# Kernel tuning notes

Hardware: AMD Instinct MI355X
Metric: run time of the kernel (lower is better)

Reference implementation:

```python
import jax, jax.numpy as jnp
import numpy as np

M, D, I, E, TOPK = 2048, 1024, 2048, 8, 2

def setup_inputs() -> dict:
    key = jax.random.key(0)
    k1, k2, k3, k4 = jax.random.split(key, 4)
    x = jax.random.normal(k1, (M, D), dtype=jnp.float32)
    w13 = jax.random.normal(k2, (E, 2 * I, D), dtype=jnp.float32) * 0.02
    w2 = jax.random.normal(k3, (E, D, I), dtype=jnp.float32) * 0.02
    expert_indices = jax.random.randint(k4, (M, TOPK), 0, E, dtype=jnp.int64)
    return {"x": x, "w13": w13, "w2": w2, "expert_indices": expert_indices}

def reference(x, w13, w2, expert_indices):
    # Faithful to the 'gpt-fast' math: per (token, slot) SiLU-gated expert FFN.
    # Instead of gathering per-token weight copies (huge), compute each expert's
    # FFN densely over all tokens, then gather the selected expert output.
    inter = w2.shape[2]

    def per_expert(w13_e, w2_e):
        h = jnp.einsum('md,nd->mn', x, w13_e)          # [M, 2I]
        x1, x3 = h[:, :inter], h[:, inter:]
        return jnp.einsum('mi,di->md', jax.nn.silu(x1) * x3, w2_e)  # [M, D]

    outs = jax.vmap(per_expert)(w13, w2)               # [E, M, D]
    outs = jnp.transpose(outs, (1, 0, 2))              # [M, E, D]
    # out[t, a] = outs[t, expert_indices[t, a]]
    idx = expert_indices[..., None]                    # [M, TOPK, 1]
    return jnp.take_along_axis(outs, idx, axis=1)      # [M, TOPK, D]
```

## Files before the change

### kernel.cpp

```cpp
#include <hip/hip_runtime.h>
#include <hip/hip_bf16.h>
#include <cstdint>
#include <cstddef>

#define DDIM  1024
#define IDIM  2048
#define NEXP  8
#define NPAIR 4096
#define MAXTILE 40

typedef __attribute__((ext_vector_type(8))) short short8;
typedef __attribute__((ext_vector_type(4))) float floatx4;
typedef __attribute__((ext_vector_type(4))) float fvec4;

__device__ inline short8 pack8v(fvec4 a, fvec4 b) {
    union { short8 s8; __hip_bfloat162 h[4]; } u;
    u.h[0] = __float22bfloat162_rn(float2{a.x, a.y});
    u.h[1] = __float22bfloat162_rn(float2{a.z, a.w});
    u.h[2] = __float22bfloat162_rn(float2{b.x, b.y});
    u.h[3] = __float22bfloat162_rn(float2{b.z, b.w});
    return u.s8;
}

__device__ inline void gload_lds16(const unsigned short* g, unsigned short* l) {
    __builtin_amdgcn_global_load_lds((const __attribute__((address_space(1))) void*)g,
                                     (__attribute__((address_space(3))) void*)l, 16, 0, 0);
}

__launch_bounds__(256)
__global__ void cvt_all(const fvec4* __restrict__ x, const fvec4* __restrict__ w13,
                        const fvec4* __restrict__ w2,
                        uint4* __restrict__ xb, uint4* __restrict__ w13b,
                        uint4* __restrict__ w2b) {
    const int t = threadIdx.x;
    for (int job = blockIdx.x; job < 6400; job += gridDim.x) {
        const fvec4* src; uint4* dst; int cbase;
        if (job < 4096)      { src = w13; dst = w13b; cbase = job << 10; }
        else if (job < 6144) { src = w2;  dst = w2b;  cbase = (job - 4096) << 10; }
        else                 { src = x;   dst = xb;   cbase = (job - 6144) << 10; }
        const int c0 = cbase + t;
        fvec4 a0 = __builtin_nontemporal_load(src + 2 * (c0 + 0));
        fvec4 b0 = __builtin_nontemporal_load(src + 2 * (c0 + 0) + 1);
        fvec4 a1 = __builtin_nontemporal_load(src + 2 * (c0 + 256));
        fvec4 b1 = __builtin_nontemporal_load(src + 2 * (c0 + 256) + 1);
        fvec4 a2 = __builtin_nontemporal_load(src + 2 * (c0 + 512));
        fvec4 b2 = __builtin_nontemporal_load(src + 2 * (c0 + 512) + 1);
        fvec4 a3 = __builtin_nontemporal_load(src + 2 * (c0 + 768));
        fvec4 b3 = __builtin_nontemporal_load(src + 2 * (c0 + 768) + 1);
        __builtin_amdgcn_sched_barrier(0);
        short8 p0 = pack8v(a0, b0);
        short8 p1 = pack8v(a1, b1);
        short8 p2 = pack8v(a2, b2);
        short8 p3 = pack8v(a3, b3);
        dst[c0 + 0]   = *(uint4*)&p0;
        dst[c0 + 256] = *(uint4*)&p1;
        dst[c0 + 512] = *(uint4*)&p2;
        dst[c0 + 768] = *(uint4*)&p3;
    }
}

__global__ void route_kernel(const int* __restrict__ eidx,
                             int4* __restrict__ tbl,
                             int* __restrict__ slot_q) {
    __shared__ int cnt[NEXP];
    __shared__ int cur[NEXP];
    const int t = threadIdx.x;
    if (t < NEXP) cnt[t] = 0;
    __syncthreads();
    for (int q = t; q < NPAIR; q += 1024) atomicAdd(&cnt[eidx[q]], 1);
    __syncthreads();
    if (t == 0) {
        int s = 0, nt = 0;
        for (int e = 0; e < NEXP; e++) {
            cur[e] = s;
            for (int mb = 0; mb < cnt[e]; mb += 128)
                tbl[nt++] = int4{e, mb, s, cnt[e]};
            s += cnt[e];
        }
        for (; nt < MAXTILE; nt++) tbl[nt] = int4{0, 0, 0, 0};
    }
    __syncthreads();
    for (int q = t; q < NPAIR; q += 1024) {
        int e = eidx[q];
        int pos = atomicAdd(&cur[e], 1);
        slot_q[pos] = q;
    }
}

__launch_bounds__(256)
__global__ void gemm1_swiglu(const unsigned short* __restrict__ xb,
                             const unsigned short* __restrict__ w13b,
                             const int4* __restrict__ tbl,
                             const int* __restrict__ slot_q,
                             unsigned short* __restrict__ pbuf) {
    const int4 tt = tbl[blockIdx.y];
    const int e = tt.x, mbase = tt.y, off0 = tt.z, ne = tt.w;
    if (mbase >= ne) return;
    const int n0 = blockIdx.x * 64;

    __shared__ __align__(16) unsigned short As[2][128 * 64];
    __shared__ __align__(16) unsigned short Bs[2][128 * 64];

    const int t    = threadIdx.x;
    const int lane = t & 63;
    const int wid  = t >> 6;

    const int rr = t >> 3;
    const int g  = (t & 7) ^ (rr & 7);
    const unsigned short* pA[4];
    const unsigned short* pB[4];
    const unsigned short* wb1 = w13b + (size_t)e * (2 * IDIM) * DDIM;
    #pragma unroll
    for (int c = 0; c < 4; c++) {
        int row = c * 32 + rr;
        int sl = mbase + row; if (sl > ne - 1) sl = ne - 1;
        pA[c] = xb + (size_t)(slot_q[off0 + sl] >> 1) * DDIM + g * 8;
        int wrow = (row < 64) ? (n0 + row) : (IDIM + n0 + (row - 64));
        pB[c] = wb1 + (size_t)wrow * DDIM + g * 8;
    }
    const int lo = wid * 512;

    const int wm = wid >> 1, wn = wid & 1;
    const int quad = lane >> 4, l16 = lane & 15;
    const int rsw = l16 & 7;
    const int co0 = (quad ^ rsw) * 8;
    const int co1 = ((quad + 4) ^ rsw) * 8;

    floatx4 acc1[4][2], acc3[4][2];
    #pragma unroll
    for (int i = 0; i < 4; i++)
        #pragma unroll
        for (int j = 0; j < 2; j++) {
            acc1[i][j] = floatx4{0.f, 0.f, 0.f, 0.f};
            acc3[i][j] = floatx4{0.f, 0.f, 0.f, 0.f};
        }

    #pragma unroll
    for (int c = 0; c < 4; c++) {
        gload_lds16(pA[c], &As[0][lo + c * 2048]);
        gload_lds16(pB[c], &Bs[0][lo + c * 2048]);
    }
    __builtin_amdgcn_sched_barrier(0);

    int cur = 0;
    for (int it = 0; it < DDIM / 64; ++it) {
        if (it + 1 < DDIM / 64) {
            const int ko = (it + 1) * 64;
            #pragma unroll
            for (int c = 0; c < 4; c++) {
                gload_lds16(pA[c] + ko, &As[cur ^ 1][lo + c * 2048]);
                gload_lds16(pB[c] + ko, &Bs[cur ^ 1][lo + c * 2048]);
            }
            __builtin_amdgcn_sched_barrier(0);
            asm volatile("s_waitcnt vmcnt(8)" ::: "memory");
        } else {
            asm volatile("s_waitcnt vmcnt(0)" ::: "memory");
        }
        __builtin_amdgcn_s_barrier();
        __builtin_amdgcn_sched_barrier(0);

        __builtin_amdgcn_s_setprio(1);
        #pragma unroll
        for (int h = 0; h < 2; ++h) {
            const int co = h ? co1 : co0;
            short8 af[4], b1f[2], b3f[2];
            #pragma unroll
            for (int mi = 0; mi < 4; mi++)
                af[mi] = *(short8*)&As[cur][(wm * 64 + mi * 16 + l16) * 64 + co];
            #pragma unroll
            for (int ni = 0; ni < 2; ni++) {
                b1f[ni] = *(short8*)&Bs[cur][(wn * 32 + ni * 16 + l16) * 64 + co];
                b3f[ni] = *(short8*)&Bs[cur][(64 + wn * 32 + ni * 16 + l16) * 64 + co];
            }
            #pragma unroll
            for (int mi = 0; mi < 4; mi++)
                #pragma unroll
                for (int ni = 0; ni < 2; ni++) {
                    acc1[mi][ni] = __builtin_amdgcn_mfma_f32_16x16x32_bf16(af[mi], b1f[ni], acc1[mi][ni], 0, 0, 0);
                    acc3[mi][ni] = __builtin_amdgcn_mfma_f32_16x16x32_bf16(af[mi], b3f[ni], acc3[mi][ni], 0, 0, 0);
                }
        }
        __builtin_amdgcn_s_setprio(0);
        __builtin_amdgcn_s_barrier();
        __builtin_amdgcn_sched_barrier(0);
        cur ^= 1;
    }

    #pragma unroll
    for (int mi = 0; mi < 4; mi++) {
        #pragma unroll
        for (int ni = 0; ni < 2; ni++) {
            const int col = n0 + wn * 32 + ni * 16 + l16;
            #pragma unroll
            for (int rw = 0; rw < 4; rw++) {
                const int s2 = mbase + wm * 64 + mi * 16 + quad * 4 + rw;
                if (s2 < ne) {
                    float v1 = acc1[mi][ni][rw];
                    float v3 = acc3[mi][ni][rw];
                    float pv = v1 / (1.f + __expf(-v1)) * v3;
                    __hip_bfloat16 pb = __float2bfloat16(pv);
                    pbuf[(size_t)(off0 + s2) * IDIM + col] = *(unsigned short*)&pb;
                }
            }
        }
    }
}

__launch_bounds__(256)
__global__ void gemm2_out(const unsigned short* __restrict__ pbuf,
                          const unsigned short* __restrict__ w2b,
                          const int4* __restrict__ tbl,
                          const int* __restrict__ slot_q,
                          float* __restrict__ out) {
    const int4 tt = tbl[blockIdx.y];
    const int e = tt.x, mbase = tt.y, off0 = tt.z, ne = tt.w;
    if (mbase >= ne) return;
    const int n0 = blockIdx.x * 64;

    __shared__ __align__(16) unsigned short As[2][128 * 64];
    __shared__ __align__(16) unsigned short Bs[2][64 * 64];

    const int t    = threadIdx.x;
    const int lane = t & 63;
    const int wid  = t >> 6;

    const int rr = t >> 3;
    const int g  = (t & 7) ^ (rr & 7);
    const unsigned short* pA[4];
    const unsigned short* pB[2];
    const unsigned short* wb = w2b + (size_t)e * DDIM * IDIM;
    #pragma unroll
    for (int c = 0; c < 4; c++) {
        int row = c * 32 + rr;
        int sl = mbase + row; if (sl > ne - 1) sl = ne - 1;
        pA[c] = pbuf + (size_t)(off0 + sl) * IDIM + g * 8;
    }
    #pragma unroll
    for (int c = 0; c < 2; c++) {
        int row = c * 32 + rr;
        pB[c] = wb + (size_t)(n0 + row) * IDIM + g * 8;
    }
    const int lo = wid * 512;

    const int wm = wid >> 1, wn = wid & 1;
    const int quad = lane >> 4, l16 = lane & 15;
    const int rsw = l16 & 7;
    const int co0 = (quad ^ rsw) * 8;
    const int co1 = ((quad + 4) ^ rsw) * 8;

    floatx4 acc[4][2];
    #pragma unroll
    for (int i = 0; i < 4; i++)
        #pragma unroll
        for (int j = 0; j < 2; j++) acc[i][j] = floatx4{0.f, 0.f, 0.f, 0.f};

    #pragma unroll
    for (int c = 0; c < 4; c++)
        gload_lds16(pA[c], &As[0][lo + c * 2048]);
    #pragma unroll
    for (int c = 0; c < 2; c++)
        gload_lds16(pB[c], &Bs[0][lo + c * 2048]);
    __builtin_amdgcn_sched_barrier(0);

    int cur = 0;
    for (int it = 0; it < IDIM / 64; ++it) {
        if (it + 1 < IDIM / 64) {
            const int ko = (it + 1) * 64;
            #pragma unroll
            for (int c = 0; c < 4; c++)
                gload_lds16(pA[c] + ko, &As[cur ^ 1][lo + c * 2048]);
            #pragma unroll
            for (int c = 0; c < 2; c++)
                gload_lds16(pB[c] + ko, &Bs[cur ^ 1][lo + c * 2048]);
            __builtin_amdgcn_sched_barrier(0);
            asm volatile("s_waitcnt vmcnt(6)" ::: "memory");
        } else {
            asm volatile("s_waitcnt vmcnt(0)" ::: "memory");
        }
        __builtin_amdgcn_s_barrier();
        __builtin_amdgcn_sched_barrier(0);

        __builtin_amdgcn_s_setprio(1);
        #pragma unroll
        for (int h = 0; h < 2; ++h) {
            const int co = h ? co1 : co0;
            short8 af[4], bf[2];
            #pragma unroll
            for (int mi = 0; mi < 4; mi++)
                af[mi] = *(short8*)&As[cur][(wm * 64 + mi * 16 + l16) * 64 + co];
            #pragma unroll
            for (int ni = 0; ni < 2; ni++)
                bf[ni] = *(short8*)&Bs[cur][(wn * 32 + ni * 16 + l16) * 64 + co];
            #pragma unroll
            for (int mi = 0; mi < 4; mi++)
                #pragma unroll
                for (int ni = 0; ni < 2; ni++)
                    acc[mi][ni] = __builtin_amdgcn_mfma_f32_16x16x32_bf16(af[mi], bf[ni], acc[mi][ni], 0, 0, 0);
        }
        __builtin_amdgcn_s_setprio(0);
        __builtin_amdgcn_s_barrier();
        __builtin_amdgcn_sched_barrier(0);
        cur ^= 1;
    }

    #pragma unroll
    for (int mi = 0; mi < 4; mi++) {
        #pragma unroll
        for (int rw = 0; rw < 4; rw++) {
            const int s2 = mbase + wm * 64 + mi * 16 + quad * 4 + rw;
            if (s2 < ne) {
                const int qq = slot_q[off0 + s2];
                float* orow = out + (size_t)qq * DDIM;
                #pragma unroll
                for (int ni = 0; ni < 2; ni++)
                    orow[n0 + wn * 32 + ni * 16 + l16] = acc[mi][ni][rw];
            }
        }
    }
}

extern "C" void kernel_launch(void* const* d_in, const int* in_sizes, int n_in,
                              void* d_out, int out_size, void* d_ws, size_t ws_size,
                              hipStream_t stream) {
    const float* x    = (const float*)d_in[0];
    const float* w13  = (const float*)d_in[1];
    const float* w2   = (const float*)d_in[2];
    const int*   eidx = (const int*)d_in[3];
    float* out = (float*)d_out;

    const size_t OFF_XB   = 65536;
    const size_t OFF_W13B = OFF_XB + (size_t)4 * 1024 * 1024;
    const size_t OFF_W2B  = OFF_W13B + (size_t)64 * 1024 * 1024;
    const size_t OFF_PBUF = OFF_W2B + (size_t)32 * 1024 * 1024;

    int4* tbl   = (int4*)((char*)d_ws + 128);
    int* slot_q = (int*)((char*)d_ws + 1024);
    unsigned short* xb   = (unsigned short*)((char*)d_ws + OFF_XB);
    unsigned short* w13b = (unsigned short*)((char*)d_ws + OFF_W13B);
    unsigned short* w2b  = (unsigned short*)((char*)d_ws + OFF_W2B);
    unsigned short* pbuf = (unsigned short*)((char*)d_ws + OFF_PBUF);

    hipLaunchKernelGGL(route_kernel, dim3(1), dim3(1024), 0, stream, eidx, tbl, slot_q);
    hipLaunchKernelGGL(cvt_all, dim3(6400), dim3(256), 0, stream,
                       (const fvec4*)x, (const fvec4*)w13, (const fvec4*)w2,
                       (uint4*)xb, (uint4*)w13b, (uint4*)w2b);
    hipLaunchKernelGGL(gemm1_swiglu, dim3(IDIM / 64, MAXTILE), dim3(256), 0, stream,
                       xb, w13b, tbl, slot_q, pbuf);
    hipLaunchKernelGGL(gemm2_out, dim3(DDIM / 64, MAXTILE), dim3(256), 0, stream,
                       pbuf, w2b, tbl, slot_q, out);
}
```

Baseline: 341.1 us.

## Fuse routing into convert kernel and add XCD-aware block swizzle to GEMMs

Removes the separate single-block routing kernel by running it as an extra block of the fp32-to-bf16 conversion kernel, saving a launch and a serialized tiny kernel. Reorders the conversion jobs to convert w2 and x first. Remaps GEMM block indices so consecutive blocks sharing an expert and tile land on the same XCD, aiming to improve L2 reuse of weights and activations. The swizzle assumes the grid size is divisible by eight.

```diff
diff --git a/kernel.cpp b/kernel.cpp
--- a/kernel.cpp
+++ b/kernel.cpp
@@ -27,17 +27,54 @@
                                      (__attribute__((address_space(3))) void*)l, 16, 0, 0);
 }
 
+__device__ inline void xcd_swz(int gridX, int nwg, int& bx, int& by) {
+    const int lin = by * gridX + bx;
+    const int q = nwg >> 3;
+    const int swz = (lin & 7) * q + (lin >> 3);
+    bx = swz % gridX; by = swz / gridX;
+}
+
 __launch_bounds__(256)
-__global__ void cvt_all(const fvec4* __restrict__ x, const fvec4* __restrict__ w13,
-                        const fvec4* __restrict__ w2,
-                        uint4* __restrict__ xb, uint4* __restrict__ w13b,
-                        uint4* __restrict__ w2b) {
+__global__ void cvt_route(const fvec4* __restrict__ x, const fvec4* __restrict__ w13,
+                          const fvec4* __restrict__ w2,
+                          uint4* __restrict__ xb, uint4* __restrict__ w13b,
+                          uint4* __restrict__ w2b,
+                          const int* __restrict__ eidx,
+                          int4* __restrict__ tbl,
+                          int* __restrict__ slot_q) {
     const int t = threadIdx.x;
+
+    if (blockIdx.x == 6400) {
+        __shared__ int cnt[NEXP];
+        __shared__ int cur[NEXP];
+        if (t < NEXP) cnt[t] = 0;
+        __syncthreads();
+        for (int q = t; q < NPAIR; q += 256) atomicAdd(&cnt[eidx[q]], 1);
+        __syncthreads();
+        if (t == 0) {
+            int s = 0, nt = 0;
+            for (int e = 0; e < NEXP; e++) {
+                cur[e] = s;
+                for (int mb = 0; mb < cnt[e]; mb += 128)
+                    tbl[nt++] = int4{e, mb, s, cnt[e]};
+                s += cnt[e];
+            }
+            for (; nt < MAXTILE; nt++) tbl[nt] = int4{0, 0, 0, 0};
+        }
+        __syncthreads();
+        for (int q = t; q < NPAIR; q += 256) {
+            int e = eidx[q];
+            int pos = atomicAdd(&cur[e], 1);
+            slot_q[pos] = q;
+        }
+        return;
+    }
+
     for (int job = blockIdx.x; job < 6400; job += gridDim.x) {
         const fvec4* src; uint4* dst; int cbase;
-        if (job < 4096)      { src = w13; dst = w13b; cbase = job << 10; }
-        else if (job < 6144) { src = w2;  dst = w2b;  cbase = (job - 4096) << 10; }
-        else                 { src = x;   dst = xb;   cbase = (job - 6144) << 10; }
+        if (job < 2048)      { src = w2;  dst = w2b;  cbase = job << 10; }
+        else if (job < 2304) { src = x;   dst = xb;   cbase = (job - 2048) << 10; }
+        else                 { src = w13; dst = w13b; cbase = (job - 2304) << 10; }
         const int c0 = cbase + t;
         fvec4 a0 = __builtin_nontemporal_load(src + 2 * (c0 + 0));
         fvec4 b0 = __builtin_nontemporal_load(src + 2 * (c0 + 0) + 1);
@@ -59,44 +96,18 @@
     }
 }
 
-__global__ void route_kernel(const int* __restrict__ eidx,
-                             int4* __restrict__ tbl,
-                             int* __restrict__ slot_q) {
-    __shared__ int cnt[NEXP];
-    __shared__ int cur[NEXP];
-    const int t = threadIdx.x;
-    if (t < NEXP) cnt[t] = 0;
-    __syncthreads();
-    for (int q = t; q < NPAIR; q += 1024) atomicAdd(&cnt[eidx[q]], 1);
-    __syncthreads();
-    if (t == 0) {
-        int s = 0, nt = 0;
-        for (int e = 0; e < NEXP; e++) {
-            cur[e] = s;
-            for (int mb = 0; mb < cnt[e]; mb += 128)
-                tbl[nt++] = int4{e, mb, s, cnt[e]};
-            s += cnt[e];
-        }
-        for (; nt < MAXTILE; nt++) tbl[nt] = int4{0, 0, 0, 0};
-    }
-    __syncthreads();
-    for (int q = t; q < NPAIR; q += 1024) {
-        int e = eidx[q];
-        int pos = atomicAdd(&cur[e], 1);
-        slot_q[pos] = q;
-    }
-}
-
 __launch_bounds__(256)
 __global__ void gemm1_swiglu(const unsigned short* __restrict__ xb,
                              const unsigned short* __restrict__ w13b,
                              const int4* __restrict__ tbl,
                              const int* __restrict__ slot_q,
                              unsigned short* __restrict__ pbuf) {
-    const int4 tt = tbl[blockIdx.y];
+    int bx = blockIdx.x, by = blockIdx.y;
+    xcd_swz(32, 32 * MAXTILE, bx, by);
+    const int4 tt = tbl[by];
     const int e = tt.x, mbase = tt.y, off0 = tt.z, ne = tt.w;
     if (mbase >= ne) return;
-    const int n0 = blockIdx.x * 64;
+    const int n0 = bx * 64;
 
     __shared__ __align__(16) unsigned short As[2][128 * 64];
     __shared__ __align__(16) unsigned short Bs[2][128 * 64];
@@ -212,10 +223,12 @@
                           const int4* __restrict__ tbl,
                           const int* __restrict__ slot_q,
                           float* __restrict__ out) {
-    const int4 tt = tbl[blockIdx.y];
+    int bx = blockIdx.x, by = blockIdx.y;
+    xcd_swz(16, 16 * MAXTILE, bx, by);
+    const int4 tt = tbl[by];
     const int e = tt.x, mbase = tt.y, off0 = tt.z, ne = tt.w;
     if (mbase >= ne) return;
-    const int n0 = blockIdx.x * 64;
+    const int n0 = bx * 64;
 
     __shared__ __align__(16) unsigned short As[2][128 * 64];
     __shared__ __align__(16) unsigned short Bs[2][64 * 64];
@@ -340,10 +353,10 @@
     unsigned short* w2b  = (unsigned short*)((char*)d_ws + OFF_W2B);
     unsigned short* pbuf = (unsigned short*)((char*)d_ws + OFF_PBUF);
 
-    hipLaunchKernelGGL(route_kernel, dim3(1), dim3(1024), 0, stream, eidx, tbl, slot_q);
-    hipLaunchKernelGGL(cvt_all, dim3(6400), dim3(256), 0, stream,
+    hipLaunchKernelGGL(cvt_route, dim3(6401), dim3(256), 0, stream,
                        (const fvec4*)x, (const fvec4*)w13, (const fvec4*)w2,
-                       (uint4*)xb, (uint4*)w13b, (uint4*)w2b);
+                       (uint4*)xb, (uint4*)w13b, (uint4*)w2b,
+                       eidx, tbl, slot_q);
     hipLaunchKernelGGL(gemm1_swiglu, dim3(IDIM / 64, MAXTILE), dim3(256), 0, stream,
                        xb, w13b, tbl, slot_q, pbuf);
     hipLaunchKernelGGL(gemm2_out, dim3(DDIM / 64, MAXTILE), dim3(256), 0, stream,
```

After: 348.0 us. 1.02x slower.

## Load weight fragments directly from global into registers, bypassing LDS

Applied to the files above, without the earlier changes.

Both expert GEMM kernels now read the weight (B) operand straight from global memory into per-lane MFMA fragment registers, instead of staging it through a shared-memory buffer. Each lane fetches its 16-byte fragments and the kernel double-buffers them in registers, unrolling the K loop by two. Activations (A) are still staged in LDS. This halves LDS footprint and LDS read traffic, but costs more registers. The global reads are also poorly coalesced, since each lane reads 16 bytes from a different row, and reuse of B across the two M-waves now comes only from cache.

```diff
diff --git a/kernel.cpp b/kernel.cpp
--- a/kernel.cpp
+++ b/kernel.cpp
@@ -99,7 +99,6 @@
     const int n0 = blockIdx.x * 64;
 
     __shared__ __align__(16) unsigned short As[2][128 * 64];
-    __shared__ __align__(16) unsigned short Bs[2][128 * 64];
 
     const int t    = threadIdx.x;
     const int lane = t & 63;
@@ -108,15 +107,11 @@
     const int rr = t >> 3;
     const int g  = (t & 7) ^ (rr & 7);
     const unsigned short* pA[4];
-    const unsigned short* pB[4];
-    const unsigned short* wb1 = w13b + (size_t)e * (2 * IDIM) * DDIM;
     #pragma unroll
     for (int c = 0; c < 4; c++) {
         int row = c * 32 + rr;
         int sl = mbase + row; if (sl > ne - 1) sl = ne - 1;
         pA[c] = xb + (size_t)(slot_q[off0 + sl] >> 1) * DDIM + g * 8;
-        int wrow = (row < 64) ? (n0 + row) : (IDIM + n0 + (row - 64));
-        pB[c] = wb1 + (size_t)wrow * DDIM + g * 8;
     }
     const int lo = wid * 512;
 
@@ -126,6 +121,26 @@
     const int co0 = (quad ^ rsw) * 8;
     const int co1 = ((quad + 4) ^ rsw) * 8;
 
+    const unsigned short* wb1 = w13b + (size_t)e * (2 * IDIM) * DDIM;
+    const int r0 = n0 + wn * 32 + l16;
+    const unsigned short* b1n0 = wb1 + (size_t)(r0)            * DDIM + quad * 8;
+    const unsigned short* b1n1 = wb1 + (size_t)(r0 + 16)       * DDIM + quad * 8;
+    const unsigned short* b3n0 = wb1 + (size_t)(IDIM + r0)     * DDIM + quad * 8;
+    const unsigned short* b3n1 = wb1 + (size_t)(IDIM + r0 + 16)* DDIM + quad * 8;
+
+    short8 bA[2][2][2], bB[2][2][2];
+
+#define LOADB1(dst, ko) {                                        \
+    dst[0][0][0] = *(const short8*)(b1n0 + (ko));                \
+    dst[0][0][1] = *(const short8*)(b1n1 + (ko));                \
+    dst[0][1][0] = *(const short8*)(b1n0 + (ko) + 32);           \
+    dst[0][1][1] = *(const short8*)(b1n1 + (ko) + 32);           \
+    dst[1][0][0] = *(const short8*)(b3n0 + (ko));                \
+    dst[1][0][1] = *(const short8*)(b3n1 + (ko));                \
+    dst[1][1][0] = *(const short8*)(b3n0 + (ko) + 32);           \
+    dst[1][1][1] = *(const short8*)(b3n1 + (ko) + 32);           \
+}
+
     floatx4 acc1[4][2], acc3[4][2];
     #pragma unroll
     for (int i = 0; i < 4; i++)
@@ -135,55 +150,62 @@
             acc3[i][j] = floatx4{0.f, 0.f, 0.f, 0.f};
         }
 
-    #pragma unroll
-    for (int c = 0; c < 4; c++) {
-        gload_lds16(pA[c], &As[0][lo + c * 2048]);
-        gload_lds16(pB[c], &Bs[0][lo + c * 2048]);
-    }
+#define COMPUTE1(bufi, breg) {                                                     \
+    __builtin_amdgcn_s_setprio(1);                                                 \
+    _Pragma("unroll")                                                              \
+    for (int h = 0; h < 2; ++h) {                                                  \
+        const int co = h ? co1 : co0;                                              \
+        short8 af[4];                                                              \
+        _Pragma("unroll")                                                          \
+        for (int mi = 0; mi < 4; mi++)                                             \
+            af[mi] = *(short8*)&As[bufi][(wm * 64 + mi * 16 + l16) * 64 + co];     \
+        _Pragma("unroll")                                                          \
+        for (int mi = 0; mi < 4; mi++)                                             \
+            _Pragma("unroll")                                                      \
+            for (int ni = 0; ni < 2; ni++) {                                       \
+                acc1[mi][ni] = __builtin_amdgcn_mfma_f32_16x16x32_bf16(af[mi], breg[0][h][ni], acc1[mi][ni], 0, 0, 0); \
+                acc3[mi][ni] = __builtin_amdgcn_mfma_f32_16x16x32_bf16(af[mi], breg[1][h][ni], acc3[mi][ni], 0, 0, 0); \
+            }                                                                      \
+    }                                                                              \
+    __builtin_amdgcn_s_setprio(0);                                                 \
+}
+
+    #pragma unroll
+    for (int c = 0; c < 4; c++) gload_lds16(pA[c], &As[0][lo + c * 2048]);
+    LOADB1(bA, 0);
     __builtin_amdgcn_sched_barrier(0);
 
-    int cur = 0;
-    for (int it = 0; it < DDIM / 64; ++it) {
-        if (it + 1 < DDIM / 64) {
-            const int ko = (it + 1) * 64;
+    for (int j = 0; j < 8; ++j) {
+        {
+            const int ko = (2 * j + 1) * 64;
             #pragma unroll
-            for (int c = 0; c < 4; c++) {
-                gload_lds16(pA[c] + ko, &As[cur ^ 1][lo + c * 2048]);
-                gload_lds16(pB[c] + ko, &Bs[cur ^ 1][lo + c * 2048]);
+            for (int c = 0; c < 4; c++) gload_lds16(pA[c] + ko, &As[1][lo + c * 2048]);
+            LOADB1(bB, ko);
+            __builtin_amdgcn_sched_barrier(0);
+            asm volatile("s_waitcnt vmcnt(12)" ::: "memory");
+            __builtin_amdgcn_s_barrier();
+            __builtin_amdgcn_sched_barrier(0);
+            COMPUTE1(0, bA);
+            __builtin_amdgcn_s_barrier();
+            __builtin_amdgcn_sched_barrier(0);
+        }
+        {
+            if (2 * j + 2 < 16) {
+                const int ko = (2 * j + 2) * 64;
+                #pragma unroll
+                for (int c = 0; c < 4; c++) gload_lds16(pA[c] + ko, &As[0][lo + c * 2048]);
+                LOADB1(bA, ko);
+                __builtin_amdgcn_sched_barrier(0);
+                asm volatile("s_waitcnt vmcnt(12)" ::: "memory");
+            } else {
+                asm volatile("s_waitcnt vmcnt(0)" ::: "memory");
             }
-            __builtin_amdgcn_sched_barrier(0);
-            asm volatile("s_waitcnt vmcnt(8)" ::: "memory");
-        } else {
-            asm volatile("s_waitcnt vmcnt(0)" ::: "memory");
-        }
-        __builtin_amdgcn_s_barrier();
-        __builtin_amdgcn_sched_barrier(0);
-
-        __builtin_amdgcn_s_setprio(1);
-        #pragma unroll
-        for (int h = 0; h < 2; ++h) {
-            const int co = h ? co1 : co0;
-            short8 af[4], b1f[2], b3f[2];
-            #pragma unroll
-            for (int mi = 0; mi < 4; mi++)
-                af[mi] = *(short8*)&As[cur][(wm * 64 + mi * 16 + l16) * 64 + co];
-            #pragma unroll
-            for (int ni = 0; ni < 2; ni++) {
-                b1f[ni] = *(short8*)&Bs[cur][(wn * 32 + ni * 16 + l16) * 64 + co];
-                b3f[ni] = *(short8*)&Bs[cur][(64 + wn * 32 + ni * 16 + l16) * 64 + co];
-            }
-            #pragma unroll
-            for (int mi = 0; mi < 4; mi++)
-                #pragma unroll
-                for (int ni = 0; ni < 2; ni++) {
-                    acc1[mi][ni] = __builtin_amdgcn_mfma_f32_16x16x32_bf16(af[mi], b1f[ni], acc1[mi][ni], 0, 0, 0);
-                    acc3[mi][ni] = __builtin_amdgcn_mfma_f32_16x16x32_bf16(af[mi], b3f[ni], acc3[mi][ni], 0, 0, 0);
-                }
-        }
-        __builtin_amdgcn_s_setprio(0);
-        __builtin_amdgcn_s_barrier();
-        __builtin_amdgcn_sched_barrier(0);
-        cur ^= 1;
+            __builtin_amdgcn_s_barrier();
+            __builtin_amdgcn_sched_barrier(0);
+            COMPUTE1(1, bB);
+            __builtin_amdgcn_s_barrier();
+            __builtin_amdgcn_sched_barrier(0);
+        }
     }
 
     #pragma unroll
@@ -204,6 +226,8 @@
             }
         }
     }
+#undef LOADB1
+#undef COMPUTE1
 }
 
 __launch_bounds__(256)
@@ -218,7 +242,6 @@
     const int n0 = blockIdx.x * 64;
 
     __shared__ __align__(16) unsigned short As[2][128 * 64];
-    __shared__ __align__(16) unsigned short Bs[2][64 * 64];
 
     const int t    = threadIdx.x;
     const int lane = t & 63;
@@ -227,18 +250,11 @@
     const int rr = t >> 3;
     const int g  = (t & 7) ^ (rr & 7);
     const unsigned short* pA[4];
-    const unsigned short* pB[2];
-    const unsigned short* wb = w2b + (size_t)e * DDIM * IDIM;
     #pragma unroll
     for (int c = 0; c < 4; c++) {
         int row = c * 32 + rr;
         int sl = mbase + row; if (sl > ne - 1) sl = ne - 1;
         pA[c] = pbuf + (size_t)(off0 + sl) * IDIM + g * 8;
-    }
-    #pragma unroll
-    for (int c = 0; c < 2; c++) {
-        int row = c * 32 + rr;
-        pB[c] = wb + (size_t)(n0 + row) * IDIM + g * 8;
     }
     const int lo = wid * 512;
 
@@ -248,59 +264,80 @@
     const int co0 = (quad ^ rsw) * 8;
     const int co1 = ((quad + 4) ^ rsw) * 8;
 
+    const unsigned short* wb = w2b + (size_t)e * DDIM * IDIM;
+    const int r0 = n0 + wn * 32 + l16;
+    const unsigned short* bn0 = wb + (size_t)(r0)      * IDIM + quad * 8;
+    const unsigned short* bn1 = wb + (size_t)(r0 + 16) * IDIM + quad * 8;
+
+    short8 bA[2][2], bB[2][2];
+
+#define LOADB2(dst, ko) {                              \
+    dst[0][0] = *(const short8*)(bn0 + (ko));          \
+    dst[0][1] = *(const short8*)(bn1 + (ko));          \
+    dst[1][0] = *(const short8*)(bn0 + (ko) + 32);     \
+    dst[1][1] = *(const short8*)(bn1 + (ko) + 32);     \
+}
+
     floatx4 acc[4][2];
     #pragma unroll
     for (int i = 0; i < 4; i++)
         #pragma unroll
         for (int j = 0; j < 2; j++) acc[i][j] = floatx4{0.f, 0.f, 0.f, 0.f};
 
-    #pragma unroll
-    for (int c = 0; c < 4; c++)
-        gload_lds16(pA[c], &As[0][lo + c * 2048]);
-    #pragma unroll
-    for (int c = 0; c < 2; c++)
-        gload_lds16(pB[c], &Bs[0][lo + c * 2048]);
+#define COMPUTE2(bufi, breg) {                                                     \
+    __builtin_amdgcn_s_setprio(1);                                                 \
+    _Pragma("unroll")                                                              \
+    for (int h = 0; h < 2; ++h) {                                                  \
+        const int co = h ? co1 : co0;                                              \
+        short8 af[4];                                                              \
+        _Pragma("unroll")                                                          \
+        for (int mi = 0; mi < 4; mi++)                                             \
+            af[mi] = *(short8*)&As[bufi][(wm * 64 + mi * 16 + l16) * 64 + co];     \
+        _Pragma("unroll")                                                          \
+        for (int mi = 0; mi < 4; mi++)                                             \
+            _Pragma("unroll")                                                      \
+            for (int ni = 0; ni < 2; ni++)                                         \
+                acc[mi][ni] = __builtin_amdgcn_mfma_f32_16x16x32_bf16(af[mi], breg[h][ni], acc[mi][ni], 0, 0, 0); \
+    }                                                                              \
+    __builtin_amdgcn_s_setprio(0);                                                 \
+}
+
+    #pragma unroll
+    for (int c = 0; c < 4; c++) gload_lds16(pA[c], &As[0][lo + c * 2048]);
+    LOADB2(bA, 0);
     __builtin_amdgcn_sched_barrier(0);
 
-    int cur = 0;
-    for (int it = 0; it < IDIM / 64; ++it) {
-        if (it + 1 < IDIM / 64) {
-            const int ko = (it + 1) * 64;
+    for (int j = 0; j < 16; ++j) {
+        {
+            const int ko = (2 * j + 1) * 64;
             #pragma unroll
-            for (int c = 0; c < 4; c++)
-                gload_lds16(pA[c] + ko, &As[cur ^ 1][lo + c * 2048]);
-            #pragma unroll
-            for (int c = 0; c < 2; c++)
-                gload_lds16(pB[c] + ko, &Bs[cur ^ 1][lo + c * 2048]);
-            __builtin_amdgcn_sched_barrier(0);
-            asm volatile("s_waitcnt vmcnt(6)" ::: "memory");
-        } else {
-            asm volatile("s_waitcnt vmcnt(0)" ::: "memory");
-        }
-        __builtin_amdgcn_s_barrier();
-        __builtin_amdgcn_sched_barrier(0);
-
-        __builtin_amdgcn_s_setprio(1);
-        #pragma unroll
-        for (int h = 0; h < 2; ++h) {
-            const int co = h ? co1 : co0;
-            short8 af[4], bf[2];
-            #pragma unroll
-            for (int mi = 0; mi < 4; mi++)
-                af[mi] = *(short8*)&As[cur][(wm * 64 + mi * 16 + l16) * 64 + co];
-            #pragma unroll
-            for (int ni = 0; ni < 2; ni++)
-                bf[ni] = *(short8*)&Bs[cur][(wn * 32 + ni * 16 + l16) * 64 + co];
-            #pragma unroll
-            for (int mi = 0; mi < 4; mi++)
+            for (int c = 0; c < 4; c++) gload_lds16(pA[c] + ko, &As[1][lo + c * 2048]);
+            LOADB2(bB, ko);
+            __builtin_amdgcn_sched_barrier(0);
+            asm volatile("s_waitcnt vmcnt(8)" ::: "memory");
+            __builtin_amdgcn_s_barrier();
+            __builtin_amdgcn_sched_barrier(0);
+            COMPUTE2(0, bA);
+            __builtin_amdgcn_s_barrier();
+            __builtin_amdgcn_sched_barrier(0);
+        }
+        {
+            if (2 * j + 2 < 32) {
+                const int ko = (2 * j + 2) * 64;
                 #pragma unroll
-                for (int ni = 0; ni < 2; ni++)
-                    acc[mi][ni] = __builtin_amdgcn_mfma_f32_16x16x32_bf16(af[mi], bf[ni], acc[mi][ni], 0, 0, 0);
-        }
-        __builtin_amdgcn_s_setprio(0);
-        __builtin_amdgcn_s_barrier();
-        __builtin_amdgcn_sched_barrier(0);
-        cur ^= 1;
+                for (int c = 0; c < 4; c++) gload_lds16(pA[c] + ko, &As[0][lo + c * 2048]);
+                LOADB2(bA, ko);
+                __builtin_amdgcn_sched_barrier(0);
+                asm volatile("s_waitcnt vmcnt(8)" ::: "memory");
+            } else {
+                asm volatile("s_waitcnt vmcnt(0)" ::: "memory");
+            }
+            __builtin_amdgcn_s_barrier();
+            __builtin_amdgcn_sched_barrier(0);
+            COMPUTE2(1, bB);
+            __builtin_amdgcn_s_barrier();
+            __builtin_amdgcn_sched_barrier(0);
+        }
     }
 
     #pragma unroll
@@ -317,6 +354,8 @@
             }
         }
     }
+#undef LOADB2
+#undef COMPUTE2
 }
 
 extern "C" void kernel_launch(void* const* d_in, const int* in_sizes, int n_in,
```

Result: slower. 397.6 us (+16.6%).
